# Optimization experiments

Hardware: AMD Instinct MI355X
Metric: run time of the kernel (lower is better)

Reference implementation:

```python
import jax, jax.numpy as jnp
import numpy as np

B, T, D, H, L, V = 2, 1024, 768, 12, 6, 50257
HS = D // H  # head_size = 64
EPS = 1e-5  # torch LayerNorm default


def _ln(x, g, b):
    m = x.mean(-1, keepdims=True)
    var = ((x - m) ** 2).mean(-1, keepdims=True)
    return (x - m) * jax.lax.rsqrt(var + EPS) * g + b


def setup_inputs() -> dict:
    key = jax.random.key(0)
    ks = jax.random.split(key, 12)
    s = 0.02  # init std per _init_weights
    n = lambda k, shape: jax.random.normal(k, shape, jnp.float32) * s
    return {
        "idx": jax.random.randint(ks[0], (B, T), 0, V),
        "tok_emb": n(ks[1], (V, D)),
        "pos_emb": n(ks[2], (T, D)),
        # per-layer stacked weights; per-head Q/K/V (bias=False in source)
        "wq": n(ks[3], (L, H, D, HS)),
        "wk": n(ks[4], (L, H, D, HS)),
        "wv": n(ks[5], (L, H, D, HS)),
        "wproj": n(ks[6], (L, D, D)),
        "bproj": jnp.zeros((L, D), jnp.float32),
        "w1": n(ks[7], (L, D, 4 * D)),
        "b1": jnp.zeros((L, 4 * D), jnp.float32),
        "w2": n(ks[8], (L, 4 * D, D)),
        "b2": jnp.zeros((L, D), jnp.float32),
        "ln1_g": jnp.ones((L, D), jnp.float32),
        "ln1_b": jnp.zeros((L, D), jnp.float32),
        "ln2_g": jnp.ones((L, D), jnp.float32),
        "ln2_b": jnp.zeros((L, D), jnp.float32),
        "lm_w": n(ks[9], (D, V)),
        "lm_b": jnp.zeros((V,), jnp.float32),
    }


def reference(idx, tok_emb, pos_emb, wq, wk, wv, wproj, bproj, w1, b1, w2,
              b2, ln1_g, ln1_b, ln2_g, ln2_b, lm_w, lm_b):
    x = tok_emb[idx] + pos_emb[None, :, :]  # [B,T,D]
    tril = jnp.tril(jnp.ones((T, T), bool))
    scale = HS ** -0.5  # k.shape[-1] ** -0.5 in source
    for l in range(L):  # small fixed layer count
        # batched per-head QKV (equivalent to the per-head Linear loop + concat)
        q = jnp.einsum('btd,hds->bhts', x, wq[l])
        k = jnp.einsum('btd,hds->bhts', x, wk[l])
        v = jnp.einsum('btd,hds->bhts', x, wv[l])
        wei = jnp.einsum('bhts,bhus->bhtu', q, k) * scale
        wei = jnp.where(tril, wei, -jnp.inf)  # causal forward_mask
        wei = jax.nn.softmax(wei, axis=-1)  # every row has >=1 valid entry
        o = jnp.einsum('bhtu,bhus->bhts', wei, v)
        o = o.transpose(0, 2, 1, 3).reshape(B, T, D)  # concat heads
        sa = o @ wproj[l] + bproj[l]
        x = _ln(x + sa, ln1_g[l], ln1_b[l])  # post-LN as in source
        h = jax.nn.relu(x @ w1[l] + b1[l]) @ w2[l] + b2[l]
        x = _ln(x + h, ln2_g[l], ln2_b[l])
    return x @ lm_w + lm_b  # logits [B,T,V]
```

## Files before the change

### kernel.cpp

```cpp
#include <hip/hip_runtime.h>

#define FLAG_RELU 1
#define FLAG_CAUSAL 2
#define FLAG_OUTF32 4

typedef __attribute__((ext_vector_type(4))) float f32x4;
typedef __attribute__((ext_vector_type(8))) short s16x8;
typedef unsigned short u16;

__device__ __forceinline__ float bf2f(u16 u) {
  union { unsigned int i; float f; } x; x.i = ((unsigned int)u) << 16; return x.f;
}
__device__ __forceinline__ u16 f2bf(float f) {
  union { float f; unsigned int i; } x; x.f = f;
  unsigned int r = (x.i + 0x7fffu + ((x.i >> 16) & 1u)) >> 16;
  return (u16)r;
}

__global__ __launch_bounds__(256) void gemm_bt(
    const u16* __restrict__ A, const u16* __restrict__ Bt, void* __restrict__ Cv,
    int M, int N, int K, int lda, int ldb, int ldc,
    int zdiv, long aS1, long aS2, long bS1, long bS2, long cS1, long cS2,
    const float* __restrict__ bias, float scale, int flags)
{
  __shared__ u16 As[128][40];
  __shared__ u16 Bs[128][40];
  int z = blockIdx.z;
  int z1 = z / zdiv, z2 = z % zdiv;
  const u16* Ab = A + z1 * aS1 + z2 * aS2 + (long)blockIdx.y * 128 * lda;
  const u16* Bb = Bt + z1 * bS1 + z2 * bS2 + (long)blockIdx.x * 128 * ldb;
  long offC = z1 * cS1 + z2 * cS2;
  int tid = threadIdx.x;
  int lane = tid & 63, wave = tid >> 6;
  int wm = (wave >> 1) << 6, wn = (wave & 1) << 6;
  int row0 = tid >> 2, cc = (tid & 3) << 3;
  int fr = lane & 15, fq = (lane >> 4) << 3;
  f32x4 acc[4][4] = {};
  for (int k0 = 0; k0 < K; k0 += 32) {
    s16x8 a0 = *(const s16x8*)(Ab + (long)row0 * lda + k0 + cc);
    s16x8 a1 = *(const s16x8*)(Ab + (long)(row0 + 64) * lda + k0 + cc);
    s16x8 b0 = *(const s16x8*)(Bb + (long)row0 * ldb + k0 + cc);
    s16x8 b1 = *(const s16x8*)(Bb + (long)(row0 + 64) * ldb + k0 + cc);
    __syncthreads();
    *(s16x8*)&As[row0][cc] = a0;
    *(s16x8*)&As[row0 + 64][cc] = a1;
    *(s16x8*)&Bs[row0][cc] = b0;
    *(s16x8*)&Bs[row0 + 64][cc] = b1;
    __syncthreads();
    s16x8 af[4], bfr[4];
#pragma unroll
    for (int i = 0; i < 4; i++) af[i] = *(const s16x8*)&As[wm + i * 16 + fr][fq];
#pragma unroll
    for (int i = 0; i < 4; i++) bfr[i] = *(const s16x8*)&Bs[wn + i * 16 + fr][fq];
#pragma unroll
    for (int mi = 0; mi < 4; mi++)
#pragma unroll
      for (int ni = 0; ni < 4; ni++)
        acc[mi][ni] = __builtin_amdgcn_mfma_f32_16x16x32_bf16(af[mi], bfr[ni], acc[mi][ni], 0, 0, 0);
  }
  int m0 = blockIdx.y * 128, n0 = blockIdx.x * 128;
  int eq = (lane >> 4) << 2;
  float* Cf = (float*)Cv;
  u16* Ch = (u16*)Cv;
#pragma unroll
  for (int ni = 0; ni < 4; ni++) {
    int c = n0 + wn + ni * 16 + fr;
    if (c >= N) continue;
    float bv = bias ? bias[c] : 0.f;
#pragma unroll
    for (int mi = 0; mi < 4; mi++) {
      int rbase = m0 + wm + mi * 16 + eq;
#pragma unroll
      for (int j = 0; j < 4; j++) {
        int r = rbase + j;
        float v = acc[mi][ni][j] * scale + bv;
        if ((flags & FLAG_RELU) && v < 0.f) v = 0.f;
        if ((flags & FLAG_CAUSAL) && c > r) v = -1e30f;
        long idx = offC + (long)r * ldc + c;
        if (flags & FLAG_OUTF32) Cf[idx] = v; else Ch[idx] = f2bf(v);
      }
    }
  }
}

__global__ __launch_bounds__(256) void transpose_f2b(
    const float* __restrict__ src, u16* __restrict__ dst,
    int R, int C, int lds_, int ldd, int Cpad, int zdiv,
    long sS1, long sS2, long dS1, long dS2)
{
  __shared__ u16 tile[32][33];
  int z = blockIdx.z;
  const float* s = src + (z / zdiv) * sS1 + (z % zdiv) * sS2;
  u16* d = dst + (z / zdiv) * dS1 + (z % zdiv) * dS2;
  int c0 = blockIdx.x * 32, r0 = blockIdx.y * 32;
  int tx = threadIdx.x & 31, ty = threadIdx.x >> 5;
#pragma unroll
  for (int i = 0; i < 32; i += 8) {
    int r = r0 + ty + i, c = c0 + tx;
    u16 v = 0;
    if (r < R && c < C) v = f2bf(s[(long)r * lds_ + c]);
    tile[ty + i][tx] = v;
  }
  __syncthreads();
#pragma unroll
  for (int i = 0; i < 32; i += 8) {
    int c = c0 + ty + i, r = r0 + tx;
    if (c < Cpad && r < R) d[(long)c * ldd + r] = tile[tx][ty + i];
  }
}

__global__ __launch_bounds__(256) void transpose_b2b(
    const u16* __restrict__ src, u16* __restrict__ dst,
    int R, int C, int lds_, int ldd, int Cpad, int zdiv,
    long sS1, long sS2, long dS1, long dS2)
{
  __shared__ u16 tile[32][33];
  int z = blockIdx.z;
  const u16* s = src + (z / zdiv) * sS1 + (z % zdiv) * sS2;
  u16* d = dst + (z / zdiv) * dS1 + (z % zdiv) * dS2;
  int c0 = blockIdx.x * 32, r0 = blockIdx.y * 32;
  int tx = threadIdx.x & 31, ty = threadIdx.x >> 5;
#pragma unroll
  for (int i = 0; i < 32; i += 8) {
    int r = r0 + ty + i, c = c0 + tx;
    u16 v = 0;
    if (r < R && c < C) v = s[(long)r * lds_ + c];
    tile[ty + i][tx] = v;
  }
  __syncthreads();
#pragma unroll
  for (int i = 0; i < 32; i += 8) {
    int c = c0 + ty + i, r = r0 + tx;
    if (c < Cpad && r < R) d[(long)c * ldd + r] = tile[tx][ty + i];
  }
}

__global__ __launch_bounds__(256) void softmax_rows(u16* __restrict__ S)
{
  __shared__ float red[8];
  long row = blockIdx.x;
  u16* p = S + row * 1024;
  int tid = threadIdx.x;
  float v[4];
  float mx = -1e30f;
#pragma unroll
  for (int i = 0; i < 4; i++) { v[i] = bf2f(p[tid + i * 256]); mx = fmaxf(mx, v[i]); }
  for (int off = 32; off >= 1; off >>= 1) mx = fmaxf(mx, __shfl_down(mx, off));
  if ((tid & 63) == 0) red[tid >> 6] = mx;
  __syncthreads();
  if (tid == 0) red[4] = fmaxf(fmaxf(red[0], red[1]), fmaxf(red[2], red[3]));
  __syncthreads();
  mx = red[4];
  float sum = 0.f;
#pragma unroll
  for (int i = 0; i < 4; i++) { v[i] = __expf(v[i] - mx); sum += v[i]; }
  for (int off = 32; off >= 1; off >>= 1) sum += __shfl_down(sum, off);
  if ((tid & 63) == 0) red[tid >> 6] = sum;
  __syncthreads();
  if (tid == 0) red[5] = red[0] + red[1] + red[2] + red[3];
  __syncthreads();
  float rs = 1.f / red[5];
#pragma unroll
  for (int i = 0; i < 4; i++) p[tid + i * 256] = f2bf(v[i] * rs);
}

__global__ __launch_bounds__(256) void add_ln(
    float* __restrict__ x, const float* __restrict__ d,
    const float* __restrict__ g, const float* __restrict__ b,
    u16* __restrict__ xb)
{
  __shared__ float red[8];
  long base = blockIdx.x * 768L;
  int tid = threadIdx.x;
  float v[3]; float s = 0.f;
#pragma unroll
  for (int i = 0; i < 3; i++) { int k = tid + i * 256; v[i] = x[base + k] + d[base + k]; s += v[i]; }
  for (int off = 32; off >= 1; off >>= 1) s += __shfl_down(s, off);
  if ((tid & 63) == 0) red[tid >> 6] = s;
  __syncthreads();
  if (tid == 0) red[4] = (red[0] + red[1] + red[2] + red[3]) * (1.f / 768.f);
  __syncthreads();
  float mean = red[4];
  float s2 = 0.f;
#pragma unroll
  for (int i = 0; i < 3; i++) { float t = v[i] - mean; s2 += t * t; }
  for (int off = 32; off >= 1; off >>= 1) s2 += __shfl_down(s2, off);
  if ((tid & 63) == 0) red[tid >> 6] = s2;
  __syncthreads();
  if (tid == 0) red[5] = rsqrtf((red[0] + red[1] + red[2] + red[3]) * (1.f / 768.f) + 1e-5f);
  __syncthreads();
  float rstd = red[5];
#pragma unroll
  for (int i = 0; i < 3; i++) {
    int k = tid + i * 256;
    float y = (v[i] - mean) * rstd * g[k] + b[k];
    x[base + k] = y; xb[base + k] = f2bf(y);
  }
}

__global__ __launch_bounds__(256) void embed_kernel(
    const int* __restrict__ idx, const float* __restrict__ tok, const float* __restrict__ pos,
    float* __restrict__ x, u16* __restrict__ xb)
{
  long row = blockIdx.x;
  int t = (int)(row & 1023);
  long tk = idx[row];
  for (int i = threadIdx.x; i < 768; i += 256) {
    float v = tok[tk * 768 + i] + pos[(long)t * 768 + i];
    x[row * 768 + i] = v;
    xb[row * 768 + i] = f2bf(v);
  }
}

extern "C" void kernel_launch(void* const* d_in, const int* in_sizes, int n_in,
                              void* d_out, int out_size, void* d_ws, size_t ws_size,
                              hipStream_t stream)
{
  const int Bb = 2, T = 1024, D = 768, H = 12, L = 6, V = 50257, HS = 64,
            M = 2048, DFF = 3072, NQ = 2304, VP = 50304;
  const int*   idx     = (const int*)d_in[0];
  const float* tok_emb = (const float*)d_in[1];
  const float* pos_emb = (const float*)d_in[2];
  const float* wq      = (const float*)d_in[3];
  const float* wk      = (const float*)d_in[4];
  const float* wv      = (const float*)d_in[5];
  const float* wproj   = (const float*)d_in[6];
  const float* bproj   = (const float*)d_in[7];
  const float* w1      = (const float*)d_in[8];
  const float* b1      = (const float*)d_in[9];
  const float* w2      = (const float*)d_in[10];
  const float* b2      = (const float*)d_in[11];
  const float* ln1g    = (const float*)d_in[12];
  const float* ln1b    = (const float*)d_in[13];
  const float* ln2g    = (const float*)d_in[14];
  const float* ln2b    = (const float*)d_in[15];
  const float* lmw     = (const float*)d_in[16];
  const float* lmb     = (const float*)d_in[17];
  float* out = (float*)d_out;
  (void)in_sizes; (void)n_in; (void)out_size; (void)ws_size;

  char* ws = (char*)d_ws;
  size_t off = 0;
  auto alloc = [&](size_t bytes) -> char* {
    char* p = ws + off; off += (bytes + 255) & ~(size_t)255; return p;
  };
  u16* wqkv_t  = (u16*)alloc((size_t)L * NQ * D * 2);
  u16* wproj_t = (u16*)alloc((size_t)L * D * D * 2);
  u16* w1_t    = (u16*)alloc((size_t)L * DFF * D * 2);
  u16* w2_t    = (u16*)alloc((size_t)L * D * DFF * 2);
  float* x     = (float*)alloc((size_t)M * D * 4);
  u16* xb      = (u16*)alloc((size_t)M * D * 2);
  char* scratch_base = ws + off;
  u16* qkv     = (u16*)alloc((size_t)M * NQ * 2);
  u16* vt      = (u16*)alloc(((size_t)Bb * H * HS * T + 64 * T) * 2);
  u16* S       = (u16*)alloc((size_t)Bb * H * T * T * 2);
  u16* attn    = (u16*)alloc((size_t)M * D * 2);
  float* tmp   = (float*)alloc((size_t)M * D * 4);
  u16* h1      = (u16*)alloc((size_t)M * DFF * 2);
  u16* lmw_t   = (u16*)scratch_base;

  dim3 blk(256);
  {
    long sS1 = (long)H * D * HS, sS2 = (long)D * HS;
    long dS1 = (long)NQ * D,     dS2 = (long)HS * D;
    transpose_f2b<<<dim3(2, 24, L * H), blk, 0, stream>>>(wq, wqkv_t,                     D, HS, HS, D, HS, H, sS1, sS2, dS1, dS2);
    transpose_f2b<<<dim3(2, 24, L * H), blk, 0, stream>>>(wk, wqkv_t + (size_t)D * D,     D, HS, HS, D, HS, H, sS1, sS2, dS1, dS2);
    transpose_f2b<<<dim3(2, 24, L * H), blk, 0, stream>>>(wv, wqkv_t + (size_t)2 * D * D, D, HS, HS, D, HS, H, sS1, sS2, dS1, dS2);
    transpose_f2b<<<dim3(24, 24, L), blk, 0, stream>>>(wproj, wproj_t, D, D, D, D, D, 1, (long)D * D, 0, (long)D * D, 0);
    transpose_f2b<<<dim3(96, 24, L), blk, 0, stream>>>(w1, w1_t, D, DFF, DFF, D, DFF, 1, (long)D * DFF, 0, (long)DFF * D, 0);
    transpose_f2b<<<dim3(24, 96, L), blk, 0, stream>>>(w2, w2_t, DFF, D, D, DFF, D, 1, (long)DFF * D, 0, (long)D * DFF, 0);
  }
  embed_kernel<<<dim3(M), blk, 0, stream>>>(idx, tok_emb, pos_emb, x, xb);

  for (int l = 0; l < L; l++) {
    gemm_bt<<<dim3(NQ / 128, M / 128, 1), blk, 0, stream>>>(
        xb, wqkv_t + (size_t)l * NQ * D, qkv, M, NQ, D, D, D, NQ,
        1, 0, 0, 0, 0, 0, 0, nullptr, 1.f, 0);
    transpose_b2b<<<dim3(2, 32, Bb * H), blk, 0, stream>>>(
        qkv + 2 * D, vt, T, HS, NQ, T, HS, H,
        (long)T * NQ, (long)HS, (long)H * HS * T, (long)HS * T);
    gemm_bt<<<dim3(T / 128, T / 128, Bb * H), blk, 0, stream>>>(
        qkv, qkv + D, S, T, T, HS, NQ, NQ, T,
        H, (long)T * NQ, (long)HS, (long)T * NQ, (long)HS, (long)H * T * T, (long)T * T,
        nullptr, 0.125f, FLAG_CAUSAL);
    softmax_rows<<<dim3(Bb * H * T), blk, 0, stream>>>(S);
    gemm_bt<<<dim3(1, T / 128, Bb * H), blk, 0, stream>>>(
        S, vt, attn, T, HS, T, T, T, D,
        H, (long)H * T * T, (long)T * T, (long)H * HS * T, (long)HS * T, (long)T * D, (long)HS,
        nullptr, 1.f, 0);
    gemm_bt<<<dim3(D / 128, M / 128, 1), blk, 0, stream>>>(
        attn, wproj_t + (size_t)l * D * D, tmp, M, D, D, D, D, D,
        1, 0, 0, 0, 0, 0, 0, bproj + (size_t)l * D, 1.f, FLAG_OUTF32);
    add_ln<<<dim3(M), blk, 0, stream>>>(x, tmp, ln1g + (size_t)l * D, ln1b + (size_t)l * D, xb);
    gemm_bt<<<dim3(DFF / 128, M / 128, 1), blk, 0, stream>>>(
        xb, w1_t + (size_t)l * DFF * D, h1, M, DFF, D, D, D, DFF,
        1, 0, 0, 0, 0, 0, 0, b1 + (size_t)l * DFF, 1.f, FLAG_RELU);
    gemm_bt<<<dim3(D / 128, M / 128, 1), blk, 0, stream>>>(
        h1, w2_t + (size_t)l * D * DFF, tmp, M, D, DFF, DFF, DFF, D,
        1, 0, 0, 0, 0, 0, 0, b2 + (size_t)l * D, 1.f, FLAG_OUTF32);
    add_ln<<<dim3(M), blk, 0, stream>>>(x, tmp, ln2g + (size_t)l * D, ln2b + (size_t)l * D, xb);
  }
  transpose_f2b<<<dim3(1572, 24, 1), blk, 0, stream>>>(lmw, lmw_t, D, V, V, D, VP, 1, 0, 0, 0, 0);
  gemm_bt<<<dim3(VP / 128, M / 128, 1), blk, 0, stream>>>(
      xb, lmw_t, out, M, V, D, D, D, V,
      1, 0, 0, 0, 0, 0, 0, lmb, 1.f, FLAG_OUTF32);
}
```

Before: 2.642 ms.

## Use direct global-to-LDS loads, XCD-aware tile remap, and skip masked causal tiles

```diff
diff --git a/kernel.cpp b/kernel.cpp
--- a/kernel.cpp
+++ b/kernel.cpp
@@ -15,6 +15,12 @@
   union { float f; unsigned int i; } x; x.f = f;
   unsigned int r = (x.i + 0x7fffu + ((x.i >> 16) & 1u)) >> 16;
   return (u16)r;
+}
+
+__device__ __forceinline__ void gl_lds16(const u16* g, u16* l) {
+  __builtin_amdgcn_global_load_lds(
+      (const __attribute__((address_space(1))) unsigned int*)g,
+      (__attribute__((address_space(3))) unsigned int*)l, 16, 0, 0);
 }
 
 __global__ __launch_bounds__(256) void gemm_bt(
@@ -23,42 +29,57 @@
     int zdiv, long aS1, long aS2, long bS1, long bS2, long cS1, long cS2,
     const float* __restrict__ bias, float scale, int flags)
 {
-  __shared__ u16 As[128][40];
-  __shared__ u16 Bs[128][40];
+  __shared__ u16 As[128][32];
+  __shared__ u16 Bs[128][32];
+  int nx = gridDim.x, ny = gridDim.y;
+  int nwg = nx * ny;
+  int orig = blockIdx.y * nx + blockIdx.x;
+  int q = nwg >> 3, r = nwg & 7;
+  int xcd = orig & 7, rest = orig >> 3;
+  int wgid = (xcd < r ? xcd * (q + 1) : r * (q + 1) + (xcd - r) * q) + rest;
+  int tx = wgid / ny, ty = wgid % ny;
+
   int z = blockIdx.z;
   int z1 = z / zdiv, z2 = z % zdiv;
-  const u16* Ab = A + z1 * aS1 + z2 * aS2 + (long)blockIdx.y * 128 * lda;
-  const u16* Bb = Bt + z1 * bS1 + z2 * bS2 + (long)blockIdx.x * 128 * ldb;
+  const u16* Ab = A + z1 * aS1 + z2 * aS2 + (long)ty * 128 * lda;
+  const u16* Bb = Bt + z1 * bS1 + z2 * bS2 + (long)tx * 128 * ldb;
   long offC = z1 * cS1 + z2 * cS2;
   int tid = threadIdx.x;
   int lane = tid & 63, wave = tid >> 6;
   int wm = (wave >> 1) << 6, wn = (wave & 1) << 6;
   int row0 = tid >> 2, cc = (tid & 3) << 3;
   int fr = lane & 15, fq = (lane >> 4) << 3;
+  int m0 = ty * 128, n0 = tx * 128;
   f32x4 acc[4][4] = {};
-  for (int k0 = 0; k0 < K; k0 += 32) {
-    s16x8 a0 = *(const s16x8*)(Ab + (long)row0 * lda + k0 + cc);
-    s16x8 a1 = *(const s16x8*)(Ab + (long)(row0 + 64) * lda + k0 + cc);
-    s16x8 b0 = *(const s16x8*)(Bb + (long)row0 * ldb + k0 + cc);
-    s16x8 b1 = *(const s16x8*)(Bb + (long)(row0 + 64) * ldb + k0 + cc);
-    __syncthreads();
-    *(s16x8*)&As[row0][cc] = a0;
-    *(s16x8*)&As[row0 + 64][cc] = a1;
-    *(s16x8*)&Bs[row0][cc] = b0;
-    *(s16x8*)&Bs[row0 + 64][cc] = b1;
-    __syncthreads();
-    s16x8 af[4], bfr[4];
-#pragma unroll
-    for (int i = 0; i < 4; i++) af[i] = *(const s16x8*)&As[wm + i * 16 + fr][fq];
-#pragma unroll
-    for (int i = 0; i < 4; i++) bfr[i] = *(const s16x8*)&Bs[wn + i * 16 + fr][fq];
-#pragma unroll
-    for (int mi = 0; mi < 4; mi++)
-#pragma unroll
-      for (int ni = 0; ni < 4; ni++)
-        acc[mi][ni] = __builtin_amdgcn_mfma_f32_16x16x32_bf16(af[mi], bfr[ni], acc[mi][ni], 0, 0, 0);
-  }
-  int m0 = blockIdx.y * 128, n0 = blockIdx.x * 128;
+  bool skip = (flags & FLAG_CAUSAL) && (n0 > m0 + 127);
+  if (!skip) {
+    const u16* a0p = Ab + (long)row0 * lda + cc;
+    const u16* a1p = a0p + 64L * lda;
+    const u16* b0p = Bb + (long)row0 * ldb + cc;
+    const u16* b1p = b0p + 64L * ldb;
+    u16* da0 = &As[0][0] + tid * 8;
+    u16* da1 = &As[0][0] + 2048 + tid * 8;
+    u16* db0 = &Bs[0][0] + tid * 8;
+    u16* db1 = &Bs[0][0] + 2048 + tid * 8;
+    for (int k0 = 0; k0 < K; k0 += 32) {
+      if (k0) __syncthreads();
+      gl_lds16(a0p + k0, da0);
+      gl_lds16(a1p + k0, da1);
+      gl_lds16(b0p + k0, db0);
+      gl_lds16(b1p + k0, db1);
+      __syncthreads();
+      s16x8 af[4], bfr[4];
+#pragma unroll
+      for (int i = 0; i < 4; i++) af[i] = *(const s16x8*)&As[wm + i * 16 + fr][fq];
+#pragma unroll
+      for (int i = 0; i < 4; i++) bfr[i] = *(const s16x8*)&Bs[wn + i * 16 + fr][fq];
+#pragma unroll
+      for (int mi = 0; mi < 4; mi++)
+#pragma unroll
+        for (int ni = 0; ni < 4; ni++)
+          acc[mi][ni] = __builtin_amdgcn_mfma_f32_16x16x32_bf16(af[mi], bfr[ni], acc[mi][ni], 0, 0, 0);
+    }
+  }
   int eq = (lane >> 4) << 2;
   float* Cf = (float*)Cv;
   u16* Ch = (u16*)Cv;
```

Result: faster. 2.521 ms (-4.6%).
